# Optimization experiments

Measured on AMD Instinct MI355X. Metric: run time of the kernel, lower is better.

Reference implementation:

```python
import jax, jax.numpy as jnp
import numpy as np

NUM_HEADS = 12
HEAD_DIM = 64
SCALE = HEAD_DIM ** -0.5


def setup_inputs() -> dict:
    key = jax.random.key(0)
    k1, k2, k3, k4, k5 = jax.random.split(key, 5)
    B, N, C = 4, 2048, NUM_HEADS * HEAD_DIM
    x = jax.random.normal(k1, (B, N, C), dtype=jnp.float32)
    W_qkv = jax.random.normal(k2, (C, 3 * C), dtype=jnp.float32) * (C ** -0.5)
    b_qkv = jax.random.normal(k3, (3 * C,), dtype=jnp.float32) * 0.02
    W_proj = jax.random.normal(k4, (C, C), dtype=jnp.float32) * (C ** -0.5)
    b_proj = jax.random.normal(k5, (C,), dtype=jnp.float32) * 0.02
    return {"x": x, "W_qkv": W_qkv, "b_qkv": b_qkv, "W_proj": W_proj, "b_proj": b_proj}


def reference(x, W_qkv, b_qkv, W_proj, b_proj):
    B, N, C = x.shape
    H, D = NUM_HEADS, HEAD_DIM
    qkv = x @ W_qkv + b_qkv                      # [B, N, 3C]
    qkv = qkv.reshape(B, N, 3, H, D)
    q = qkv[:, :, 0].transpose(0, 2, 1, 3) * SCALE  # [B, H, N, D]
    k = qkv[:, :, 1].transpose(0, 2, 1, 3)          # [B, H, N, D]
    v = qkv[:, :, 2].transpose(0, 2, 1, 3)          # [B, H, N, D]
    attn = jnp.einsum("bhnd,bhmd->bhnm", q, k)   # [B, H, N, N]
    attn = jax.nn.softmax(attn, axis=-1)
    ctx = jnp.einsum("bhnm,bhmd->bhnd", attn, v)  # [B, H, N, D]
    attn_out = ctx.transpose(0, 2, 1, 3).reshape(B, N, C)
    out = attn_out @ W_proj + b_proj
    return (out, attn_out)
```

## Files before the change

kernel.cpp:

```cpp
#include <hip/hip_runtime.h>
#include <stdint.h>

typedef unsigned short u16;
using bf16x8 = __attribute__((ext_vector_type(8))) __bf16;
using s16x8  = __attribute__((ext_vector_type(8))) short;
using f32x4  = __attribute__((ext_vector_type(4))) float;

#define SCALE_Q 0.125f
#define LOG2E 1.44269504088896f

__device__ __forceinline__ u16 f2bf(float f) {
  union { float f; uint32_t u; } v; v.f = f;
  uint32_t u = v.u;
  return (u16)((u + 0x7FFFu + ((u >> 16) & 1)) >> 16);
}

__device__ __forceinline__ bf16x8 ld_frag(const u16* p) {
  return __builtin_bit_cast(bf16x8, *(const s16x8*)p);
}

__device__ __forceinline__ f32x4 MF(bf16x8 a, bf16x8 b, f32x4 c) {
  return __builtin_amdgcn_mfma_f32_16x16x32_bf16(a, b, c, 0, 0, 0);
}

__device__ __forceinline__ void gld16(const u16* g, u16* l) {
  __builtin_amdgcn_global_load_lds(
      (const __attribute__((address_space(1))) uint32_t*)g,
      (__attribute__((address_space(3))) uint32_t*)l, 16, 0, 0);
}

__device__ __forceinline__ uint32_t pk_bf16(float a, float b) {
  uint32_t u0 = __builtin_bit_cast(uint32_t, a) + 0x8000u;
  uint32_t u1 = __builtin_bit_cast(uint32_t, b) + 0x8000u;
  return __builtin_amdgcn_perm(u1, u0, 0x07060302u);
}

__global__ void prep_kernel(const float* __restrict__ x, u16* __restrict__ xb,
                            const float* __restrict__ Wq, u16* __restrict__ wqt,
                            const float* __restrict__ Wp, u16* __restrict__ wpt) {
  __shared__ float tile[32][33];
  int bx = blockIdx.x;
  if (bx < 6144) {
    int i = (bx * 256 + threadIdx.x) * 4;
    float4 v = *(const float4*)(x + i);
    uint2 o;
    o.x = (uint32_t)f2bf(v.x) | ((uint32_t)f2bf(v.y) << 16);
    o.y = (uint32_t)f2bf(v.z) | ((uint32_t)f2bf(v.w) << 16);
    *(uint2*)(xb + i) = o;
    return;
  }
  bx -= 6144;
  const float* in;
  u16* out;
  int C, cb, rb;
  const int R = 768;
  if (bx < 1728) { in = Wq; out = wqt; C = 2304; cb = bx % 72; rb = bx / 72; }
  else { bx -= 1728; in = Wp; out = wpt; C = 768; cb = bx % 24; rb = bx / 24; }
  int c0 = cb * 32, r0 = rb * 32;
  int tx = threadIdx.x & 31, ty = threadIdx.x >> 5;
#pragma unroll
  for (int j = 0; j < 32; j += 8)
    tile[ty + j][tx] = in[(size_t)(r0 + ty + j) * C + c0 + tx];
  __syncthreads();
#pragma unroll
  for (int j = 0; j < 32; j += 8)
    out[(size_t)(c0 + ty + j) * R + r0 + tx] = f2bf(tile[tx][ty + j]);
}

__global__ __launch_bounds__(256) void gemm_qkv(
    const u16* __restrict__ A, const u16* __restrict__ Bt, const float* __restrict__ bias,
    u16* __restrict__ q_out, u16* __restrict__ k_out, u16* __restrict__ v_out) {
  constexpr int K = 768;
  __shared__ __align__(16) u16 smem[17408];
  u16* sA = smem;
  u16* sB = smem + 8192;
  const int tid = threadIdx.x;
  const int lane = tid & 63, wave = tid >> 6;
  const int ml = lane & 15, kg = lane >> 4;
  const int wr = wave >> 1, wc = wave & 1;
  const int bid0 = blockIdx.x + blockIdx.y * 18;
  const int nbid = (bid0 & 7) * 144 + (bid0 >> 3);
  const int bn = nbid % 18, bm = nbid / 18;

  f32x4 acc[4][4] = {};
  const u16* Abase = A + (size_t)(bm * 128) * K;
  const u16* Bbase = Bt + (size_t)(bn * 128) * K;

  for (int k0 = 0; k0 < K; k0 += 64) {
#pragma unroll
    for (int p = 0; p < 4; p++) {
      int q = p * 256 + tid;
      int r = q >> 3, s = q & 7, c = s ^ (r & 7);
      gld16(Abase + (size_t)r * K + k0 + c * 8, sA + q * 8);
      gld16(Bbase + (size_t)r * K + k0 + c * 8, sB + q * 8);
    }
    __syncthreads();
#pragma unroll
    for (int kc = 0; kc < 2; kc++) {
      bf16x8 af[4], bfr[4];
      int ac = kc * 4 + kg;
#pragma unroll
      for (int i = 0; i < 4; i++) {
        int arow = wr * 64 + i * 16 + ml;
        af[i] = ld_frag(sA + (arow * 8 + (ac ^ (arow & 7))) * 8);
        int brow = wc * 64 + i * 16 + ml;
        bfr[i] = ld_frag(sB + (brow * 8 + (ac ^ (brow & 7))) * 8);
      }
#pragma unroll
      for (int mi = 0; mi < 4; mi++)
#pragma unroll
        for (int ni = 0; ni < 4; ni++)
          acc[mi][ni] = MF(af[mi], bfr[ni], acc[mi][ni]);
    }
    __syncthreads();
  }

  if (bn >= 12) {
    uint32_t* t32 = (uint32_t*)smem;
#pragma unroll
    for (int ni = 0; ni < 4; ni++) {
      int n_local = wc * 64 + ni * 16 + ml;
      float bv = bias[bn * 128 + n_local];
#pragma unroll
      for (int mi = 0; mi < 4; mi++) {
        int mh = wr * 32 + mi * 8 + kg * 2;
        t32[n_local * 68 + mh]     = pk_bf16(acc[mi][ni][0] + bv, acc[mi][ni][1] + bv);
        t32[n_local * 68 + mh + 1] = pk_bf16(acc[mi][ni][2] + bv, acc[mi][ni][3] + bv);
      }
    }
    __syncthreads();
    int row = tid >> 1, seg = tid & 1;
    int dg = (bn - 12) * 128 + row;
    int h = dg >> 6, d = dg & 63;
    int bi = bm >> 4, tok0 = (bm & 15) * 128;
    u16* dst = v_out + ((size_t)(bi * 12 + h) * 64 + d) * 2048 + tok0 + seg * 64;
    const uint32_t* srow = t32 + row * 68;
#pragma unroll
    for (int j = 0; j < 8; j++) {
      int m8 = seg * 8 + j;
      int c = m8 >> 2, k = m8 & 3;
      const uint32_t* s = srow + 16 * c + 2 * k;
      uint4 u; u.x = s[0]; u.y = s[1]; u.z = s[8]; u.w = s[9];
      *(uint4*)(dst + j * 8) = u;
    }
  } else {
    u16* dst = (bn < 6) ? q_out : k_out;
    float scl = (bn < 6) ? SCALE_Q * LOG2E : 1.0f;
#pragma unroll
    for (int ni = 0; ni < 4; ni++) {
      int n = bn * 128 + wc * 64 + ni * 16 + ml;
      int rem = (bn < 6) ? n : n - 768;
      int h = rem >> 6, d = rem & 63;
      float bv = bias[n];
#pragma unroll
      for (int mi = 0; mi < 4; mi++) {
        int m0 = bm * 128 + wr * 64 + mi * 16 + kg * 4;
#pragma unroll
        for (int r = 0; r < 4; r++) {
          int m = m0 + r;
          int bi = m >> 11, tok = m & 2047;
          dst[(size_t)(bi * 12 + h) * 131072 + (size_t)tok * 64 + d] = f2bf((acc[mi][ni][r] + bv) * scl);
        }
      }
    }
  }
}

__global__ __launch_bounds__(256) void gemm_proj(
    const u16* __restrict__ A, const u16* __restrict__ Bt, const float* __restrict__ bias,
    float* __restrict__ c_out) {
  constexpr int K = 768;
  __shared__ __align__(16) u16 sA[128 * 64];
  __shared__ __align__(16) u16 sB[64 * 64];
  const int tid = threadIdx.x;
  const int lane = tid & 63, wave = tid >> 6;
  const int ml = lane & 15, kg = lane >> 4;
  const int bid0 = blockIdx.x + blockIdx.y * 12;
  const int nbid = (bid0 & 7) * 96 + (bid0 >> 3);
  const int bn = nbid % 12, bm = nbid / 12;
  f32x4 acc[2][4] = {};
  const u16* Abase = A + (size_t)(bm * 128) * K;
  const u16* Bbase = Bt + (size_t)(bn * 64) * K;

  for (int k0 = 0; k0 < K; k0 += 64) {
#pragma unroll
    for (int p = 0; p < 4; p++) {
      int q = p * 256 + tid;
      int r = q >> 3, s = q & 7, c = s ^ (r & 7);
      gld16(Abase + (size_t)r * K + k0 + c * 8, sA + q * 8);
    }
#pragma unroll
    for (int p = 0; p < 2; p++) {
      int q = p * 256 + tid;
      int r = q >> 3, s = q & 7, c = s ^ (r & 7);
      gld16(Bbase + (size_t)r * K + k0 + c * 8, sB + q * 8);
    }
    __syncthreads();
#pragma unroll
    for (int kc = 0; kc < 2; kc++) {
      int ac = kc * 4 + kg;
      bf16x8 af[2], bfr[4];
#pragma unroll
      for (int i = 0; i < 2; i++) {
        int arow = wave * 32 + i * 16 + ml;
        af[i] = ld_frag(sA + (arow * 8 + (ac ^ (arow & 7))) * 8);
      }
#pragma unroll
      for (int i = 0; i < 4; i++) {
        int brow = i * 16 + ml;
        bfr[i] = ld_frag(sB + (brow * 8 + (ac ^ (brow & 7))) * 8);
      }
#pragma unroll
      for (int mi = 0; mi < 2; mi++)
#pragma unroll
        for (int ni = 0; ni < 4; ni++)
          acc[mi][ni] = MF(af[mi], bfr[ni], acc[mi][ni]);
    }
    __syncthreads();
  }
#pragma unroll
  for (int ni = 0; ni < 4; ni++) {
    int n = bn * 64 + ni * 16 + ml;
    float bv = bias[n];
#pragma unroll
    for (int mi = 0; mi < 2; mi++) {
      int m0 = bm * 128 + wave * 32 + mi * 16 + kg * 4;
#pragma unroll
      for (int r = 0; r < 4; r++)
        c_out[(size_t)(m0 + r) * 768 + n] = acc[mi][ni][r] + bv;
    }
  }
}

__global__ __launch_bounds__(256, 3) void attn_kernel(
    const u16* __restrict__ qs, const u16* __restrict__ ks, const u16* __restrict__ vt,
    float* __restrict__ attn_f32, u16* __restrict__ attn_bf) {
  __shared__ __align__(16) u16 sK[2][4096];
  __shared__ __align__(16) u16 sV[2][4096];
  const int tid = threadIdx.x, lane = tid & 63, wave = tid >> 6;
  const int ml = lane & 15, kg = lane >> 4;
  const int m7 = ml & 7;
  const int bid  = blockIdx.x + (blockIdx.y << 4);
  const int slot = bid >> 3;
  const int bh   = (bid & 7) * 6 + (slot >> 4);
  const int q0   = (slot & 15) * 128 + wave * 32;
  const size_t base = (size_t)bh * 131072;

  bf16x8 qf[2][2];
#pragma unroll
  for (int qt = 0; qt < 2; qt++) {
    const u16* qp = qs + base + (size_t)(q0 + qt * 16 + ml) * 64 + kg * 8;
    qf[qt][0] = ld_frag(qp);
    qf[qt][1] = ld_frag(qp + 32);
  }
  uint4 uo; uo.x = uo.y = uo.z = uo.w = 0x3F803F80u;
  const bf16x8 onesf = __builtin_bit_cast(bf16x8, uo);
  f32x4 lacc[2] = {};
  f32x4 O[2][4] = {};

  const u16* kbase[2] = { &sK[0][ml * 64 + ((0 + kg) ^ m7) * 8],
                          &sK[0][ml * 64 + ((4 + kg) ^ m7) * 8] };
  const u16* vbase[2] = { &sV[0][ml * 64 + ((0 + kg) ^ m7) * 8],
                          &sV[0][ml * 64 + ((4 + kg) ^ m7) * 8] };

  const int r0 = tid >> 3,          c0 = (tid & 7) ^ (r0 & 7);
  const int r1 = (256 + tid) >> 3,  c1 = (tid & 7) ^ (r1 & 7);
  const u16* kgp0 = ks + base + r0 * 64 + c0 * 8;
  const u16* kgp1 = ks + base + r1 * 64 + c1 * 8;
  const u16* vgp0 = vt + base + r0 * 2048 + c0 * 8;
  const u16* vgp1 = vt + base + r1 * 2048 + c1 * 8;

  auto stage = [&](int b, int kt) {
    gld16(kgp0 + kt * 64, &sK[b][tid * 8]);
    gld16(kgp1 + kt * 64, &sK[b][2048 + tid * 8]);
    gld16(vgp0 + kt,      &sV[b][tid * 8]);
    gld16(vgp1 + kt,      &sV[b][2048 + tid * 8]);
  };

  stage(0, 0);
  for (int kt = 0; kt < 2048; kt += 128) {
#pragma unroll
    for (int half = 0; half < 2; half++) {
      const int cur = kt + half * 64;
      __syncthreads();
      if (cur + 64 < 2048) stage(half ^ 1, cur + 64);

      f32x4 sc[2][4] = {};
#pragma unroll
      for (int nt = 0; nt < 4; nt++)
#pragma unroll
        for (int kc = 0; kc < 2; kc++) {
          bf16x8 kf = ld_frag(kbase[kc] + nt * 1024 + half * 4096);
          sc[0][nt] = MF(kf, qf[0][kc], sc[0][nt]);
          sc[1][nt] = MF(kf, qf[1][kc], sc[1][nt]);
        }

      bf16x8 pf[2][2];
#pragma unroll
      for (int qt = 0; qt < 2; qt++)
#pragma unroll
        for (int c = 0; c < 2; c++) {
          f32x4 pa, pb;
#pragma unroll
          for (int r = 0; r < 4; r++) {
            pa[r] = __builtin_amdgcn_exp2f(sc[qt][2 * c][r]);
            pb[r] = __builtin_amdgcn_exp2f(sc[qt][2 * c + 1][r]);
          }
          uint4 u;
          u.x = pk_bf16(pa[0], pa[1]);
          u.y = pk_bf16(pa[2], pa[3]);
          u.z = pk_bf16(pb[0], pb[1]);
          u.w = pk_bf16(pb[2], pb[3]);
          pf[qt][c] = __builtin_bit_cast(bf16x8, u);
        }

      lacc[0] = MF(pf[0][0], onesf, lacc[0]);
      lacc[0] = MF(pf[0][1], onesf, lacc[0]);
      lacc[1] = MF(pf[1][0], onesf, lacc[1]);
      lacc[1] = MF(pf[1][1], onesf, lacc[1]);

#pragma unroll
      for (int c = 0; c < 2; c++)
#pragma unroll
        for (int nt2 = 0; nt2 < 4; nt2++) {
          bf16x8 vf = ld_frag(vbase[c] + nt2 * 1024 + half * 4096);
          O[0][nt2] = MF(pf[0][c], vf, O[0][nt2]);
          O[1][nt2] = MF(pf[1][c], vf, O[1][nt2]);
        }
    }
  }

  int b = bh / 12, h = bh - b * 12;
#pragma unroll
  for (int qt = 0; qt < 2; qt++)
#pragma unroll
    for (int r = 0; r < 4; r++) {
      float inv = __builtin_amdgcn_rcpf(lacc[qt][r]);
      int qrow = q0 + qt * 16 + kg * 4 + r;
      size_t rowoff = ((size_t)(b * 2048 + qrow)) * 768 + h * 64;
#pragma unroll
      for (int nt2 = 0; nt2 < 4; nt2++) {
        float v = O[qt][nt2][r] * inv;
        int d = nt2 * 16 + ml;
        attn_f32[rowoff + d] = v;
        attn_bf[rowoff + d] = f2bf(v);
      }
    }
}

extern "C" void kernel_launch(void* const* d_in, const int* in_sizes, int n_in,
                              void* d_out, int out_size, void* d_ws, size_t ws_size,
                              hipStream_t stream) {
  const float* x      = (const float*)d_in[0];
  const float* W_qkv  = (const float*)d_in[1];
  const float* b_qkv  = (const float*)d_in[2];
  const float* W_proj = (const float*)d_in[3];
  const float* b_proj = (const float*)d_in[4];
  float* out      = (float*)d_out;
  float* attn_out = out + (size_t)8192 * 768;

  char* ws = (char*)d_ws;
  const size_t SZ_XB = (size_t)8192 * 768 * 2;
  u16* xb      = (u16*)(ws);
  u16* wqkv_t  = (u16*)(ws + SZ_XB);
  u16* wproj_t = (u16*)(ws + SZ_XB + 3538944);
  u16* qs      = (u16*)(ws + SZ_XB + 3538944 + 1179648);
  u16* ks      = (u16*)((char*)qs + SZ_XB);
  u16* vt      = (u16*)((char*)ks + SZ_XB);
  u16* ab      = xb;

  prep_kernel<<<6144 + 1728 + 576, 256, 0, stream>>>(x, xb, W_qkv, wqkv_t, W_proj, wproj_t);
  gemm_qkv<<<dim3(18, 64), 256, 0, stream>>>(xb, wqkv_t, b_qkv, qs, ks, vt);
  attn_kernel<<<dim3(16, 48), 256, 0, stream>>>(qs, ks, vt, attn_out, ab);
  gemm_proj<<<dim3(12, 64), 256, 0, stream>>>(ab, wproj_t, b_proj, out);
}
```

Baseline: 217.7 us.

## Split attention work across eight waves with sixteen query rows each

The attention kernel now launches 512 threads per block, so each of eight waves handles a 16-row query tile instead of 32 rows across two tiles. Per-thread register state (Q fragments, score and output accumulators) halves, and the K/V tile staging needs one global-to-LDS load per thread instead of two. The goal is more resident waves for latency hiding. The cost is that each K/V fragment read from LDS now feeds only one MFMA instead of two, which doubles LDS read traffic per unit of compute.

```diff
diff --git a/kernel.cpp b/kernel.cpp
--- a/kernel.cpp
+++ b/kernel.cpp
@@ -232,7 +232,7 @@
   }
 }
 
-__global__ __launch_bounds__(256, 3) void attn_kernel(
+__global__ __launch_bounds__(512, 6) void attn_kernel(
     const u16* __restrict__ qs, const u16* __restrict__ ks, const u16* __restrict__ vt,
     float* __restrict__ attn_f32, u16* __restrict__ attn_bf) {
   __shared__ __align__(16) u16 sK[2][4096];
@@ -243,38 +243,32 @@
   const int bid  = blockIdx.x + (blockIdx.y << 4);
   const int slot = bid >> 3;
   const int bh   = (bid & 7) * 6 + (slot >> 4);
-  const int q0   = (slot & 15) * 128 + wave * 32;
+  const int q0   = (slot & 15) * 128 + wave * 16;
   const size_t base = (size_t)bh * 131072;
 
-  bf16x8 qf[2][2];
-#pragma unroll
-  for (int qt = 0; qt < 2; qt++) {
-    const u16* qp = qs + base + (size_t)(q0 + qt * 16 + ml) * 64 + kg * 8;
-    qf[qt][0] = ld_frag(qp);
-    qf[qt][1] = ld_frag(qp + 32);
+  bf16x8 qf[2];
+  {
+    const u16* qp = qs + base + (size_t)(q0 + ml) * 64 + kg * 8;
+    qf[0] = ld_frag(qp);
+    qf[1] = ld_frag(qp + 32);
   }
   uint4 uo; uo.x = uo.y = uo.z = uo.w = 0x3F803F80u;
   const bf16x8 onesf = __builtin_bit_cast(bf16x8, uo);
-  f32x4 lacc[2] = {};
-  f32x4 O[2][4] = {};
+  f32x4 lacc = {};
+  f32x4 O[4] = {};
 
   const u16* kbase[2] = { &sK[0][ml * 64 + ((0 + kg) ^ m7) * 8],
                           &sK[0][ml * 64 + ((4 + kg) ^ m7) * 8] };
   const u16* vbase[2] = { &sV[0][ml * 64 + ((0 + kg) ^ m7) * 8],
                           &sV[0][ml * 64 + ((4 + kg) ^ m7) * 8] };
 
-  const int r0 = tid >> 3,          c0 = (tid & 7) ^ (r0 & 7);
-  const int r1 = (256 + tid) >> 3,  c1 = (tid & 7) ^ (r1 & 7);
-  const u16* kgp0 = ks + base + r0 * 64 + c0 * 8;
-  const u16* kgp1 = ks + base + r1 * 64 + c1 * 8;
-  const u16* vgp0 = vt + base + r0 * 2048 + c0 * 8;
-  const u16* vgp1 = vt + base + r1 * 2048 + c1 * 8;
+  const int r0 = tid >> 3, c0 = (tid & 7) ^ (r0 & 7);
+  const u16* kgp = ks + base + r0 * 64 + c0 * 8;
+  const u16* vgp = vt + base + r0 * 2048 + c0 * 8;
 
   auto stage = [&](int b, int kt) {
-    gld16(kgp0 + kt * 64, &sK[b][tid * 8]);
-    gld16(kgp1 + kt * 64, &sK[b][2048 + tid * 8]);
-    gld16(vgp0 + kt,      &sV[b][tid * 8]);
-    gld16(vgp1 + kt,      &sV[b][2048 + tid * 8]);
+    gld16(kgp + kt * 64, &sK[b][tid * 8]);
+    gld16(vgp + kt,      &sV[b][tid * 8]);
   };
 
   stage(0, 0);
@@ -285,67 +279,59 @@
       __syncthreads();
       if (cur + 64 < 2048) stage(half ^ 1, cur + 64);
 
-      f32x4 sc[2][4] = {};
+      f32x4 sc[4] = {};
 #pragma unroll
       for (int nt = 0; nt < 4; nt++)
 #pragma unroll
         for (int kc = 0; kc < 2; kc++) {
           bf16x8 kf = ld_frag(kbase[kc] + nt * 1024 + half * 4096);
-          sc[0][nt] = MF(kf, qf[0][kc], sc[0][nt]);
-          sc[1][nt] = MF(kf, qf[1][kc], sc[1][nt]);
+          sc[nt] = MF(kf, qf[kc], sc[nt]);
         }
 
-      bf16x8 pf[2][2];
-#pragma unroll
-      for (int qt = 0; qt < 2; qt++)
-#pragma unroll
-        for (int c = 0; c < 2; c++) {
-          f32x4 pa, pb;
-#pragma unroll
-          for (int r = 0; r < 4; r++) {
-            pa[r] = __builtin_amdgcn_exp2f(sc[qt][2 * c][r]);
-            pb[r] = __builtin_amdgcn_exp2f(sc[qt][2 * c + 1][r]);
-          }
-          uint4 u;
-          u.x = pk_bf16(pa[0], pa[1]);
-          u.y = pk_bf16(pa[2], pa[3]);
-          u.z = pk_bf16(pb[0], pb[1]);
-          u.w = pk_bf16(pb[2], pb[3]);
-          pf[qt][c] = __builtin_bit_cast(bf16x8, u);
+      bf16x8 pf[2];
+#pragma unroll
+      for (int c = 0; c < 2; c++) {
+        f32x4 pa, pb;
+#pragma unroll
+        for (int r = 0; r < 4; r++) {
+          pa[r] = __builtin_amdgcn_exp2f(sc[2 * c][r]);
+          pb[r] = __builtin_amdgcn_exp2f(sc[2 * c + 1][r]);
         }
-
-      lacc[0] = MF(pf[0][0], onesf, lacc[0]);
-      lacc[0] = MF(pf[0][1], onesf, lacc[0]);
-      lacc[1] = MF(pf[1][0], onesf, lacc[1]);
-      lacc[1] = MF(pf[1][1], onesf, lacc[1]);
+        uint4 u;
+        u.x = pk_bf16(pa[0], pa[1]);
+        u.y = pk_bf16(pa[2], pa[3]);
+        u.z = pk_bf16(pb[0], pb[1]);
+        u.w = pk_bf16(pb[2], pb[3]);
+        pf[c] = __builtin_bit_cast(bf16x8, u);
+      }
+
+      lacc = MF(pf[0], onesf, lacc);
+      lacc = MF(pf[1], onesf, lacc);
 
 #pragma unroll
       for (int c = 0; c < 2; c++)
 #pragma unroll
         for (int nt2 = 0; nt2 < 4; nt2++) {
           bf16x8 vf = ld_frag(vbase[c] + nt2 * 1024 + half * 4096);
-          O[0][nt2] = MF(pf[0][c], vf, O[0][nt2]);
-          O[1][nt2] = MF(pf[1][c], vf, O[1][nt2]);
+          O[nt2] = MF(pf[c], vf, O[nt2]);
         }
     }
   }
 
   int b = bh / 12, h = bh - b * 12;
 #pragma unroll
-  for (int qt = 0; qt < 2; qt++)
-#pragma unroll
-    for (int r = 0; r < 4; r++) {
-      float inv = __builtin_amdgcn_rcpf(lacc[qt][r]);
-      int qrow = q0 + qt * 16 + kg * 4 + r;
-      size_t rowoff = ((size_t)(b * 2048 + qrow)) * 768 + h * 64;
-#pragma unroll
-      for (int nt2 = 0; nt2 < 4; nt2++) {
-        float v = O[qt][nt2][r] * inv;
-        int d = nt2 * 16 + ml;
-        attn_f32[rowoff + d] = v;
-        attn_bf[rowoff + d] = f2bf(v);
-      }
-    }
+  for (int r = 0; r < 4; r++) {
+    float inv = __builtin_amdgcn_rcpf(lacc[r]);
+    int qrow = q0 + kg * 4 + r;
+    size_t rowoff = ((size_t)(b * 2048 + qrow)) * 768 + h * 64;
+#pragma unroll
+    for (int nt2 = 0; nt2 < 4; nt2++) {
+      float v = O[nt2][r] * inv;
+      int d = nt2 * 16 + ml;
+      attn_f32[rowoff + d] = v;
+      attn_bf[rowoff + d] = f2bf(v);
+    }
+  }
 }
 
 extern "C" void kernel_launch(void* const* d_in, const int* in_sizes, int n_in,
@@ -371,6 +357,6 @@
 
   prep_kernel<<<6144 + 1728 + 576, 256, 0, stream>>>(x, xb, W_qkv, wqkv_t, W_proj, wproj_t);
   gemm_qkv<<<dim3(18, 64), 256, 0, stream>>>(xb, wqkv_t, b_qkv, qs, ks, vt);
-  attn_kernel<<<dim3(16, 48), 256, 0, stream>>>(qs, ks, vt, attn_out, ab);
+  attn_kernel<<<dim3(16, 48), 512, 0, stream>>>(qs, ks, vt, attn_out, ab);
   gemm_proj<<<dim3(12, 64), 256, 0, stream>>>(ab, wproj_t, b_proj, out);
 }
```

Result: no change. 217.7 us (-0.0%).
